# Kernel tuning notes

Measured on AMD Instinct MI355X. Metric: run time of the kernel, lower is better.

Reference implementation:

```python
import jax, jax.numpy as jnp
import numpy as np

B, T, DIM = 4, 1024, 2048
N_HEADS, N_KV_HEADS = 32, 8
HEAD_DIM = DIM // N_HEADS  # 64
N_REPS = N_HEADS // N_KV_HEADS  # 4


def setup_inputs() -> dict:
    key = jax.random.key(0)
    ks = jax.random.split(key, 8)
    # RoPE tables: theta = 10000^{-2i/d}, positions 0..T-1
    inv_freq = 1.0 / (10000.0 ** (jnp.arange(0, HEAD_DIM, 2, dtype=jnp.float32) / HEAD_DIM))
    angles = jnp.arange(T, dtype=jnp.float32)[:, None] * inv_freq[None, :]  # (T, HEAD_DIM//2)
    s = 0.02
    return {
        "input": jax.random.normal(ks[0], (B, T, DIM), jnp.float32),
        "freqs_cos": jnp.cos(angles),
        "freqs_sin": jnp.sin(angles),
        "mask": jnp.tril(jnp.ones((T, T), dtype=bool)),  # causal boolean mask
        "wq": s * jax.random.normal(ks[1], (DIM, DIM), jnp.float32),
        "wk": s * jax.random.normal(ks[2], (N_KV_HEADS * HEAD_DIM, DIM), jnp.float32),
        "wv": s * jax.random.normal(ks[3], (N_KV_HEADS * HEAD_DIM, DIM), jnp.float32),
        "wo": s * jax.random.normal(ks[4], (DIM, DIM), jnp.float32),
        "curr_pos": 0,
    }


def _apply_rope(x, cos, sin):
    # x: (B, T, H, D); cos/sin: (T, D//2). Complex multiply on (even, odd) pairs.
    xr = x[..., 0::2]
    xi = x[..., 1::2]
    c = cos[None, :, None, :]
    s = sin[None, :, None, :]
    out_r = xr * c - xi * s
    out_i = xr * s + xi * c
    return jnp.stack([out_r, out_i], axis=-1).reshape(x.shape)


def reference(input, freqs_cos, freqs_sin, mask, wq, wk, wv, wo, curr_pos):
    Bv, Tv = input.shape[0], input.shape[1]
    qs = (input @ wq.T).reshape(Bv, Tv, N_HEADS, HEAD_DIM)
    ks = (input @ wk.T).reshape(Bv, Tv, N_KV_HEADS, HEAD_DIM)
    vs = (input @ wv.T).reshape(Bv, Tv, N_KV_HEADS, HEAD_DIM)
    qs = _apply_rope(qs, freqs_cos, freqs_sin)
    ks = _apply_rope(ks, freqs_cos, freqs_sin)

    # KV cache (prefill path: curr_pos == 0, fresh cache of length 2T)
    kv_cache = jnp.zeros((Bv, 2 * Tv, N_KV_HEADS, HEAD_DIM, 2), input.dtype)
    kv_cache = kv_cache.at[:, curr_pos:curr_pos + Tv, :, :, 0].set(ks)
    kv_cache = kv_cache.at[:, curr_pos:curr_pos + Tv, :, :, 1].set(vs)
    k_all = kv_cache[:, :curr_pos + Tv, :, :, 0]
    v_all = kv_cache[:, :curr_pos + Tv, :, :, 1]

    # GQA: broadcast each kv head across its query-head group (avoid repeat_interleave copy)
    S = k_all.shape[1]
    q = qs.transpose(0, 2, 1, 3).reshape(Bv, N_KV_HEADS, N_REPS, Tv, HEAD_DIM)
    k = k_all.transpose(0, 2, 1, 3)  # (B, KVH, S, D)
    v = v_all.transpose(0, 2, 1, 3)

    scale = 1.0 / jnp.sqrt(jnp.asarray(HEAD_DIM, input.dtype))
    scores = jnp.einsum("bgrqd,bgkd->bgrqk", q, k) * scale  # (B, KVH, REPS, T, S)
    neg = jnp.asarray(jnp.finfo(input.dtype).min, input.dtype)
    scores = jnp.where(mask[None, None, None, :, :S], scores, neg)
    attn = jax.nn.softmax(scores, axis=-1)
    out = jnp.einsum("bgrqk,bgkd->bgrqd", attn, v)
    out = out.reshape(Bv, N_HEADS, Tv, HEAD_DIM).transpose(0, 2, 1, 3).reshape(Bv, Tv, DIM)
    return out @ wo.T
```

## Files before the change

kernel.cpp:

```cpp
#include <hip/hip_runtime.h>
#include <cstdint>

typedef __bf16 bf16x8 __attribute__((ext_vector_type(8)));
typedef float  f32x4  __attribute__((ext_vector_type(4)));
typedef float  f32x16 __attribute__((ext_vector_type(16)));
typedef float  float8v __attribute__((ext_vector_type(8)));
typedef unsigned short ushort8v __attribute__((ext_vector_type(8)));
typedef unsigned short ushort4v __attribute__((ext_vector_type(4)));
typedef unsigned int   uint4v   __attribute__((ext_vector_type(4)));

__device__ __forceinline__ unsigned short f2b(float f) {
  uint32_t u = __builtin_bit_cast(uint32_t, f);
  u += 0x7FFFu + ((u >> 16) & 1u);
  return (unsigned short)(u >> 16);
}
__device__ __forceinline__ float b2f(unsigned short h) {
  uint32_t u = ((uint32_t)h) << 16;
  return __builtin_bit_cast(float, u);
}
__device__ __forceinline__ unsigned int cvtpk(float lo, float hi_) {
  unsigned int r;
  asm("v_cvt_pk_bf16_f32 %0, %1, %2" : "=v"(r) : "v"(lo), "v"(hi_));
  return r;
}

__device__ __forceinline__ void async16(const void* g, void* l) {
  __builtin_amdgcn_global_load_lds(
      (const __attribute__((address_space(1))) void*)g,
      (__attribute__((address_space(3))) void*)l, 16, 0, 0);
}

#define WAITVM(N)  __builtin_amdgcn_s_waitcnt(0x0F70 | ((N) & 15))

struct CvtArgs {
  const float* src[5];
  unsigned short* dst[5];
  long n[5];
};
__global__ void cvt5_kernel(CvtArgs a) {
  long base = (long)blockIdx.x * blockDim.x + threadIdx.x;
  long gstride = (long)gridDim.x * blockDim.x;
#pragma unroll 1
  for (int sg = 0; sg < 5; ++sg) {
    const float* s = a.src[sg];
    unsigned short* d = a.dst[sg];
    long n8 = a.n[sg] >> 3;
    for (long i = base; i < n8; i += gstride) {
      float8v f = *(const float8v*)(s + i * 8);
      ushort8v o;
#pragma unroll
      for (int j = 0; j < 8; ++j) o[j] = f2b(f[j]);
      *(ushort8v*)(d + i * 8) = o;
    }
  }
}

__global__ __launch_bounds__(512, 2)
void gemmQ192(const unsigned short* __restrict__ Ag, const unsigned short* __restrict__ Wg,
              unsigned short* __restrict__ Cp) {
  constexpr int K = 2048;
  constexpr int NF = 3;
  constexpr int ASLOT = 16384;
  constexpr int BSLOT = 24576;
  constexpr int N = 3072;

  extern __shared__ char lds_c[];

  const int tid = threadIdx.x;
  const int wave = tid >> 6, lane = tid & 63;
  const int wm = wave >> 2, wn = wave & 3;
  const int lr = lane & 15, lg = lane >> 4;

  const int flat = blockIdx.y * 16 + blockIdx.x;
  const int swz = (flat & 7) * 32 + (flat >> 3);
  const int m0 = (swz >> 4) * 256, n0 = (swz & 15) * 192;

  const int laneSw = (lr >> 1) * 128 + (((((lr & 1) << 2) | lg) ^ (lr >> 1)) << 4);
  const int aoff = wm * 8192 + laneSw;

  int bByte[NF], bR7[NF];
#pragma unroll
  for (int ni = 0; ni < NF; ++ni) {
    int row = wn * 48 + ni * 16 + lr;
    bByte[ni] = row * 128;
    bR7[ni] = row & 7;
  }

  f32x4 acc[8][NF] = {};
  bf16x8 af[4], bf[NF];

  auto stA = [&](int slot, int s) {
    char* sl = lds_c + slot * ASLOT;
    const int kc = s * 32;
#pragma unroll
    for (int j = 0; j < 2; ++j) {
      int q = (tid + 512 * j) * 16;
      int R = q >> 7, g2L = ((q >> 4) & 7) ^ (R & 7);
      int row = R * 2 + (g2L >> 2), kg = g2L & 3;
      async16(Ag + (size_t)(m0 + row) * K + kc + kg * 8, sl + q);
    }
  };
  auto stB = [&](int slot, int T) {
    char* sl = lds_c + 4 * ASLOT + slot * BSLOT;
    const int kc = T * 64;
#pragma unroll
    for (int j = 0; j < 3; ++j) {
      int q = (tid + 512 * j) * 16;
      int row = q >> 7, c = (q >> 4) & 7;
      async16(Wg + (size_t)(n0 + row) * K + kc + ((c ^ (row & 7)) * 8), sl + q);
    }
  };

#define PH(SA, SB, MH, KH, RDB, STG, VM)                                      \
  {                                                                           \
    const char* As_ = lds_c + (SA) * ASLOT;                                   \
    _Pragma("unroll") for (int mi = 0; mi < 4; ++mi)                          \
      af[mi] = *(const bf16x8*)(As_ + aoff + ((MH) * 4 + mi) * 1024);         \
    if (RDB) {                                                                \
      const char* Bs_ = lds_c + 4 * ASLOT + (SB) * BSLOT;                     \
      _Pragma("unroll") for (int ni = 0; ni < NF; ++ni)                       \
        bf[ni] = *(const bf16x8*)(Bs_ + bByte[ni] +                           \
                                  (((((KH) << 2) | lg) ^ bR7[ni]) << 4));     \
    }                                                                         \
    STG;                                                                      \
    if ((VM) >= 0) WAITVM(VM);                                                \
    __builtin_amdgcn_s_barrier();                                             \
    __builtin_amdgcn_s_setprio(1);                                            \
    _Pragma("unroll") for (int mi = 0; mi < 4; ++mi)                          \
      _Pragma("unroll") for (int ni = 0; ni < NF; ++ni)                       \
        acc[(MH) * 4 + mi][ni] = __builtin_amdgcn_mfma_f32_16x16x32_bf16(     \
            af[mi], bf[ni], acc[(MH) * 4 + mi][ni], 0, 0, 0);                 \
    __builtin_amdgcn_s_setprio(0);                                            \
    __builtin_amdgcn_s_barrier();                                             \
  }

  stB(0, 0); stA(0, 0); stA(1, 1); stB(1, 1); stA(2, 2);
  WAITVM(5);
  __builtin_amdgcn_s_barrier();

  for (int t2 = 0; t2 < 30; t2 += 2) {
    PH(0, 0, 0, 0, true,  stA(3, 2 * t2 + 3), -1);
    PH(0, 0, 1, 0, false, (void)0, -1);
    PH(1, 0, 0, 1, true,  stA(0, 2 * t2 + 4), -1);
    PH(1, 0, 1, 1, false, stB(0, t2 + 2), 5);
    PH(2, 1, 0, 0, true,  stA(1, 2 * t2 + 5), -1);
    PH(2, 1, 1, 0, false, (void)0, -1);
    PH(3, 1, 0, 1, true,  stA(2, 2 * t2 + 6), -1);
    PH(3, 1, 1, 1, false, stB(1, t2 + 3), 5);
  }
  PH(0, 0, 0, 0, true,  stA(3, 63), -1);
  PH(0, 0, 1, 0, false, (void)0, -1);
  PH(1, 0, 0, 1, true,  (void)0, -1);
  PH(1, 0, 1, 1, false, (void)0, 0);
  PH(2, 1, 0, 0, true,  (void)0, -1);
  PH(2, 1, 1, 0, false, (void)0, -1);
  PH(3, 1, 0, 1, true,  (void)0, -1);
  PH(3, 1, 1, 1, false, (void)0, -1);
#undef PH

#pragma unroll
  for (int mig = 0; mig < 8; ++mig) {
#pragma unroll
    for (int j = 0; j < 4; ++j) {
      int row = m0 + wm * 128 + mig * 16 + lg * 4 + j;
#pragma unroll
      for (int ni = 0; ni < NF; ++ni) {
        int col = n0 + wn * 48 + ni * 16 + lr;
        Cp[(size_t)row * N + col] = f2b(acc[mig][ni][j]);
      }
    }
  }
}

template<bool F32OUT, int BN, int GX, int GY>
__global__ __launch_bounds__(512, 2)
void gemm8p(const unsigned short* __restrict__ Ag, const unsigned short* __restrict__ Wg,
            void* __restrict__ Cp, int N) {
  constexpr int K = 2048;
  constexpr int BM = 256;
  constexpr int NF = BN / 64;
  constexpr int AL = 2;
  constexpr int BL = BN / 128;
  constexpr int VMS = 2 * BL + AL;
  constexpr int ASLOT = BM * 64;
  constexpr int BSLOT = BN * 64;
  constexpr int NWG = GX * GY;
  constexpr int CPX = NWG / 8;

  extern __shared__ char lds_c[];

  const int tid = threadIdx.x;
  const int wave = tid >> 6, lane = tid & 63;
  const int wm = wave >> 2, wn = wave & 3;
  const int lr = lane & 15, lg = lane >> 4;

  const int flat = blockIdx.y * GX + blockIdx.x;
  const int swz = (flat & 7) * CPX + (flat >> 3);
  const int m0 = (swz / GX) * BM, n0 = (swz % GX) * BN;

  const int laneSw = (lr >> 1) * 128 + (((((lr & 1) << 2) | lg) ^ (lr >> 1)) << 4);
  const int aoff = wm * 128 * 64 + laneSw;
  const int boff = wn * NF * 1024 + laneSw;

  f32x4 acc[8][NF] = {};
  bf16x8 af[4], bf[NF];

  auto stA = [&](int slot, int s) {
    char* sl = lds_c + slot * ASLOT;
    const int kc = s * 32;
#pragma unroll
    for (int j = 0; j < AL; ++j) {
      int q = (tid + 512 * j) * 16;
      int R = q >> 7, g2L = ((q >> 4) & 7) ^ (R & 7);
      int row = R * 2 + (g2L >> 2), kg = g2L & 3;
      async16(Ag + (size_t)(m0 + row) * K + kc + kg * 8, sl + q);
    }
  };
  auto stB = [&](int slot, int s) {
    char* sl = lds_c + 4 * ASLOT + slot * BSLOT;
    const int kc = s * 32;
#pragma unroll
    for (int j = 0; j < BL; ++j) {
      int q = (tid + 512 * j) * 16;
      int R = q >> 7, g2L = ((q >> 4) & 7) ^ (R & 7);
      int row = R * 2 + (g2L >> 2), kg = g2L & 3;
      async16(Wg + (size_t)(n0 + row) * K + kc + kg * 8, sl + q);
    }
  };

#define PH(RSLOT, MH, RDB, STG, VM)                                           \
  {                                                                           \
    const char* As_ = lds_c + (RSLOT) * ASLOT;                                \
    _Pragma("unroll") for (int mi = 0; mi < 4; ++mi)                          \
      af[mi] = *(const bf16x8*)(As_ + aoff + ((MH) * 4 + mi) * 1024);         \
    if (RDB) {                                                                \
      const char* Bs_ = lds_c + 4 * ASLOT + (RSLOT) * BSLOT;                  \
      _Pragma("unroll") for (int ni = 0; ni < NF; ++ni)                       \
        bf[ni] = *(const bf16x8*)(Bs_ + boff + ni * 1024);                    \
    }                                                                         \
    STG;                                                                      \
    if ((VM) >= 0) WAITVM(VM);                                                \
    __builtin_amdgcn_s_barrier();                                             \
    __builtin_amdgcn_s_setprio(1);                                            \
    _Pragma("unroll") for (int mi = 0; mi < 4; ++mi)                          \
      _Pragma("unroll") for (int ni = 0; ni < NF; ++ni)                       \
        acc[(MH) * 4 + mi][ni] = __builtin_amdgcn_mfma_f32_16x16x32_bf16(     \
            af[mi], bf[ni], acc[(MH) * 4 + mi][ni], 0, 0, 0);                 \
    __builtin_amdgcn_s_setprio(0);                                            \
    __builtin_amdgcn_s_barrier();                                             \
  }

  stB(0, 0); stA(0, 0); stB(1, 1); stA(1, 1); stB(2, 2); stA(2, 2); stB(3, 3);
  WAITVM(VMS);
  __builtin_amdgcn_s_barrier();

  for (int T = 0; T < 30; T += 2) {
    const int p0 = 2 * T;
    PH(0, 0, true,  stA(3, p0 + 3), -1);
    PH(0, 1, false, stB(0, p0 + 4), -1);
    PH(1, 0, true,  stA(0, p0 + 4), -1);
    PH(1, 1, false, stB(1, p0 + 5), VMS);
    PH(2, 0, true,  stA(1, p0 + 5), -1);
    PH(2, 1, false, stB(2, p0 + 6), -1);
    PH(3, 0, true,  stA(2, p0 + 6), -1);
    PH(3, 1, false, stB(3, p0 + 7), VMS);
  }
  PH(0, 0, true,  stA(3, 63), -1);
  PH(0, 1, false, (void)0, -1);
  PH(1, 0, true,  (void)0, -1);
  PH(1, 1, false, (void)0, 0);
  PH(2, 0, true,  (void)0, -1);
  PH(2, 1, false, (void)0, -1);
  PH(3, 0, true,  (void)0, -1);
  PH(3, 1, false, (void)0, -1);
#undef PH

#pragma unroll
  for (int mig = 0; mig < 8; ++mig) {
#pragma unroll
    for (int j = 0; j < 4; ++j) {
      int row = m0 + wm * 128 + mig * 16 + lg * 4 + j;
#pragma unroll
      for (int ni = 0; ni < NF; ++ni) {
        int col = n0 + wn * (NF * 16) + ni * 16 + lr;
        float v = acc[mig][ni][j];
        if (F32OUT) ((float*)Cp)[(size_t)row * N + col] = v;
        else        ((unsigned short*)Cp)[(size_t)row * N + col] = f2b(v);
      }
    }
  }
}

__global__ __launch_bounds__(256)
void ropekv_kernel(unsigned short* __restrict__ qkv,
                   const float* __restrict__ cosb, const float* __restrict__ sinb,
                   unsigned short* __restrict__ vt) {
  const int tt0 = blockIdx.x * 64;
  const int kvh = blockIdx.y;
  const int b   = blockIdx.z;
  const int tid = threadIdx.x;

  {
    int r = tid >> 2, c0 = (tid & 3) * 16;
    int t = tt0 + r;
    unsigned short* kp = qkv + (size_t)(b * 1024 + t) * 3072 + 2048 + kvh * 64 + c0;
    const float* cb = cosb + t * 32 + c0 / 2;
    const float* sb = sinb + t * 32 + c0 / 2;
    ushort8v x0 = *(const ushort8v*)kp;
    ushort8v x1 = *(const ushort8v*)(kp + 8);
    float8v c = *(const float8v*)cb;
    float8v s = *(const float8v*)sb;
    ushort8v o0, o1;
#pragma unroll
    for (int j = 0; j < 4; ++j) {
      float xr = b2f(x0[2 * j]), xi = b2f(x0[2 * j + 1]);
      o0[2 * j]     = f2b(xr * c[j] - xi * s[j]);
      o0[2 * j + 1] = f2b(xr * s[j] + xi * c[j]);
    }
#pragma unroll
    for (int j = 0; j < 4; ++j) {
      float xr = b2f(x1[2 * j]), xi = b2f(x1[2 * j + 1]);
      o1[2 * j]     = f2b(xr * c[4 + j] - xi * s[4 + j]);
      o1[2 * j + 1] = f2b(xr * s[4 + j] + xi * c[4 + j]);
    }
    *(ushort8v*)kp = o0;
    *(ushort8v*)(kp + 8) = o1;
  }

  __shared__ unsigned short lT[64 * 68];
#pragma unroll
  for (int i = 0; i < 2; ++i) {
    int r = i * 32 + (tid >> 3), c = (tid & 7) * 8;
    const unsigned short* src = qkv + (size_t)(b * 1024 + tt0 + r) * 3072 + 2560 + kvh * 64 + c;
    ushort8v v = *(const ushort8v*)src;
    ushort4v a, b4;
#pragma unroll
    for (int j = 0; j < 4; ++j) { a[j] = v[j]; b4[j] = v[j + 4]; }
    *(ushort4v*)&lT[r * 68 + c]     = a;
    *(ushort4v*)&lT[r * 68 + c + 4] = b4;
  }
  __syncthreads();
#pragma unroll
  for (int i = 0; i < 2; ++i) {
    int d = tid & 63;
    int tt = i * 4 + (tid >> 6);
    ushort8v o;
#pragma unroll
    for (int j = 0; j < 8; ++j) o[j] = lT[(tt * 8 + j) * 68 + d];
    *(ushort8v*)&vt[((size_t)((b * 8 + kvh) * 64 + d)) * 1024 + tt0 + tt * 8] = o;
  }
}

__global__ __launch_bounds__(512, 4)
void attn_kernel(const unsigned short* __restrict__ qkv, const unsigned short* __restrict__ vt,
                 const float* __restrict__ cosb, const float* __restrict__ sinb,
                 unsigned short* __restrict__ ob) {
  const int flat = (blockIdx.z * 8 + blockIdx.y) * 16 + blockIdx.x;
  const int swzb = (flat & 7) * 64 + (flat >> 3);
  const int bx = swzb & 15, kvh = (swzb >> 4) & 7, b = swzb >> 7;

  const int tid = threadIdx.x, wave = tid >> 6, lane = tid & 63;
  const int l31 = lane & 31, hi = lane >> 5;
  const int wq = wave & 3, wh = wave >> 2;
  const int h = kvh * 4 + wq;

  const int qth = 31 - bx, qtl = bx;
  const int nth = qth / 2 + 1, ntl = qtl / 2 + 1;
  const int q0 = (wh ? qtl : qth) * 32;
  const int nt = wh ? ntl : nth;

  __shared__ unsigned short lK[2][64 * 64];
  __shared__ unsigned short lVt[2][64 * 64];

  const float SC = 0.125f * 1.44269504f;
  bf16x8 qf[4];
  {
    int t = q0 + l31;
    const unsigned short* qp = qkv + (size_t)(b * 1024 + t) * 3072 + h * 64;
#pragma unroll
    for (int dk = 0; dk < 4; ++dk) {
      ushort8v q = *(const ushort8v*)(qp + dk * 16 + hi * 8);
      f32x4 c4 = *(const f32x4*)(cosb + t * 32 + dk * 8 + hi * 4);
      f32x4 s4 = *(const f32x4*)(sinb + t * 32 + dk * 8 + hi * 4);
      ushort8v o;
#pragma unroll
      for (int j = 0; j < 4; ++j) {
        float xr = b2f(q[2 * j]), xi = b2f(q[2 * j + 1]);
        o[2 * j]     = f2b((xr * c4[j] - xi * s4[j]) * SC);
        o[2 * j + 1] = f2b((xr * s4[j] + xi * c4[j]) * SC);
      }
      qf[dk] = __builtin_bit_cast(bf16x8, o);
    }
  }

  const unsigned short* kg = qkv + (size_t)(b * 1024) * 3072 + 2048 + kvh * 64;
  const unsigned short* vg = vt + (size_t)(b * 8 + kvh) * 64 * 1024;

  auto stage = [&](int kvb, int bi) {
    const int sr  = tid >> 3;
    const int scb = (tid & 7) * 16;
    {
      int cb = scb ^ ((sr & 7) << 4);
      async16(kg + (size_t)(kvb + sr) * 3072 + (cb >> 1), &lK[bi][sr * 64 + (scb >> 1)]);
    }
    {
      int cbv = scb ^ ((sr & 7) << 4);
      async16(vg + (size_t)sr * 1024 + kvb + (cbv >> 1), &lVt[bi][sr * 64 + (scb >> 1)]);
    }
  };

  f32x16 oacc[2] = {};
  float m2 = -3e38f, l_run = 0.f;

  auto chunk64 = [&](int cur, int ckvb, bool lastT) {
    f32x16 sd[2] = {};
    __builtin_amdgcn_s_setprio(1);
#pragma unroll
    for (int s = 0; s < 2; ++s) {
      const int krow = s * 32 + l31;
      const char* kr = (const char*)lK[cur] + krow * 128;
      const int swz = (krow & 7) << 4;
#pragma unroll
      for (int dk = 0; dk < 4; ++dk) {
        bf16x8 kf = *(const bf16x8*)(kr + ((dk * 32 + hi * 16) ^ swz));
        sd[s] = __builtin_amdgcn_mfma_f32_32x32x16_bf16(kf, qf[dk], sd[s], 0, 0, 0);
      }
    }
    __builtin_amdgcn_s_setprio(0);

    if (lastT) {
#pragma unroll
      for (int s = 0; s < 2; ++s)
#pragma unroll
        for (int r = 0; r < 16; ++r) {
          int kvg = ckvb + s * 32 + (r & 3) + 8 * (r >> 2) + 4 * hi;
          if (kvg > q0 + l31) sd[s][r] = -3e38f;
        }
    }
    float pm = sd[0][0];
#pragma unroll
    for (int s = 0; s < 2; ++s)
#pragma unroll
      for (int r = 0; r < 16; ++r) pm = fmaxf(pm, sd[s][r]);
    pm = fmaxf(pm, __shfl_xor(pm, 32));
    if (!__all(pm <= m2 + 11.0f)) {
      float mnew = fmaxf(m2, pm);
      float alpha = exp2f(m2 - mnew);
      m2 = mnew;
      l_run *= alpha;
#pragma unroll
      for (int db = 0; db < 2; ++db)
#pragma unroll
        for (int r = 0; r < 16; ++r) oacc[db][r] *= alpha;
    }
    float tsum = 0.f;
#pragma unroll
    for (int s = 0; s < 2; ++s)
#pragma unroll
      for (int r = 0; r < 16; ++r) { float p = exp2f(sd[s][r] - m2); sd[s][r] = p; tsum += p; }
    tsum += __shfl_xor(tsum, 32);
    l_run += tsum;

    bf16x8 pf[2][2];
#pragma unroll
    for (int s = 0; s < 2; ++s)
#pragma unroll
      for (int kc = 0; kc < 2; ++kc) {
        unsigned int cA = cvtpk(sd[s][8 * kc + 0], sd[s][8 * kc + 1]);
        unsigned int cB = cvtpk(sd[s][8 * kc + 4], sd[s][8 * kc + 5]);
        unsigned int cC = cvtpk(sd[s][8 * kc + 2], sd[s][8 * kc + 3]);
        unsigned int cD = cvtpk(sd[s][8 * kc + 6], sd[s][8 * kc + 7]);
        unsigned int xA = __shfl_xor(cA, 32), xB = __shfl_xor(cB, 32);
        unsigned int xC = __shfl_xor(cC, 32), xD = __shfl_xor(cD, 32);
        uint4v u;
        u[0] = hi ? xB : cA;
        u[1] = hi ? xD : cC;
        u[2] = hi ? cB : xA;
        u[3] = hi ? cD : xC;
        pf[s][kc] = __builtin_bit_cast(bf16x8, u);
      }

    __builtin_amdgcn_s_setprio(1);
#pragma unroll
    for (int db = 0; db < 2; ++db) {
      const int row = db * 32 + l31;
      const char* vr = (const char*)lVt[cur] + row * 128;
      const int vswz = (row & 7) << 4;
#pragma unroll
      for (int s = 0; s < 2; ++s)
#pragma unroll
        for (int kc = 0; kc < 2; ++kc) {
          bf16x8 vf = *(const bf16x8*)(vr + ((s * 64 + kc * 32 + hi * 16) ^ vswz));
          oacc[db] = __builtin_amdgcn_mfma_f32_32x32x16_bf16(vf, pf[s][kc], oacc[db], 0, 0, 0);
        }
    }
    __builtin_amdgcn_s_setprio(0);
  };

  stage(0, 0);
  __syncthreads();

  for (int j = 0; j < nth; ++j) {
    const int cur = j & 1;
    if (j + 1 < nth) stage((j + 1) * 64, cur ^ 1);
    if (j < nt) chunk64(cur, j * 64, j == nt - 1);
    __syncthreads();
  }

  {
    float inv = 1.0f / l_run;
    unsigned short* orow = ob + (size_t)(b * 1024 + q0 + l31) * 2048 + h * 64;
#pragma unroll
    for (int db = 0; db < 2; ++db)
#pragma unroll
      for (int g = 0; g < 4; ++g) {
        int d0 = db * 32 + 8 * g + 4 * hi;
        ushort4v o;
#pragma unroll
        for (int j = 0; j < 4; ++j) o[j] = f2b(oacc[db][4 * g + j] * inv);
        *(ushort4v*)(orow + d0) = o;
      }
  }
}

extern "C" void kernel_launch(void* const* d_in, const int* in_sizes, int n_in,
                              void* d_out, int out_size, void* d_ws, size_t ws_size,
                              hipStream_t stream) {
  const float* input = (const float*)d_in[0];
  const float* fcos  = (const float*)d_in[1];
  const float* fsin  = (const float*)d_in[2];
  const float* wq = (const float*)d_in[4];
  const float* wk = (const float*)d_in[5];
  const float* wv = (const float*)d_in[6];
  const float* wo = (const float*)d_in[7];
  float* out = (float*)d_out;

  unsigned short* xb   = (unsigned short*)d_ws;
  unsigned short* wqkv = xb + (size_t)4096 * 2048;
  unsigned short* wob  = wqkv + (size_t)3072 * 2048;
  unsigned short* qkv  = wob + (size_t)2048 * 2048;
  unsigned short* ob   = qkv + (size_t)4096 * 3072;
  unsigned short* vtb  = xb;

  hipFuncSetAttribute((const void*)&gemmQ192,
                      hipFuncAttributeMaxDynamicSharedMemorySize, 114688);
  hipFuncSetAttribute((const void*)&gemm8p<true, 128, 16, 16>,
                      hipFuncAttributeMaxDynamicSharedMemorySize, 98304);

  CvtArgs ca;
  ca.src[0] = input; ca.dst[0] = xb;                        ca.n[0] = (long)4096 * 2048;
  ca.src[1] = wq;    ca.dst[1] = wqkv;                      ca.n[1] = (long)2048 * 2048;
  ca.src[2] = wk;    ca.dst[2] = wqkv + (size_t)2048 * 2048; ca.n[2] = (long)512 * 2048;
  ca.src[3] = wv;    ca.dst[3] = wqkv + (size_t)2560 * 2048; ca.n[3] = (long)512 * 2048;
  ca.src[4] = wo;    ca.dst[4] = wob;                       ca.n[4] = (long)2048 * 2048;
  hipLaunchKernelGGL(cvt5_kernel, dim3(2048), dim3(256), 0, stream, ca);

  hipLaunchKernelGGL(gemmQ192, dim3(16, 16), dim3(512), 114688,
                     stream, xb, wqkv, qkv);

  hipLaunchKernelGGL(ropekv_kernel, dim3(16, 8, 4), dim3(256), 0, stream,
                     qkv, fcos, fsin, vtb);

  hipLaunchKernelGGL(attn_kernel, dim3(16, 8, 4), dim3(512), 0, stream,
                     qkv, vtb, fcos, fsin, ob);

  hipLaunchKernelGGL((gemm8p<true, 128, 16, 16>), dim3(16, 16), dim3(512), 98304,
                     stream, ob, wob, (void*)out, 2048);
}
```

Baseline: 157.0 us.

## Halve GEMM M-tile to 128 rows and unify both projections in one template

Replaces the QKV GEMM and the output GEMM with one templated kernel that uses 128-row tiles instead of 256, doubling the grid to 512 workgroups. LDS per block drops and launch bounds go to 4 blocks per CU, so more waves can hide latency and the 256 CUs get better wave coverage. In exchange, per-block operand reuse falls and B-tile traffic per FLOP doubles. The output GEMM also moves from its old pipeline variant to the QKV-style B-loading scheme.

```diff
diff --git a/kernel.cpp b/kernel.cpp
--- a/kernel.cpp
+++ b/kernel.cpp
@@ -55,14 +55,17 @@
   }
 }
 
-__global__ __launch_bounds__(512, 2)
-void gemmQ192(const unsigned short* __restrict__ Ag, const unsigned short* __restrict__ Wg,
-              unsigned short* __restrict__ Cp) {
+template<bool F32OUT, int BN>
+__global__ __launch_bounds__(512, 4)
+void gemmLT(const unsigned short* __restrict__ Ag, const unsigned short* __restrict__ Wg,
+            void* __restrict__ Cp) {
   constexpr int K = 2048;
-  constexpr int NF = 3;
-  constexpr int ASLOT = 16384;
-  constexpr int BSLOT = 24576;
-  constexpr int N = 3072;
+  constexpr int NF = BN / 64;
+  constexpr int BL = NF;
+  constexpr int VMS = 1 + BL;
+  constexpr int ASLOT = 8192;
+  constexpr int BSLOT = BN * 128;
+  constexpr int N = 16 * BN;
 
   extern __shared__ char lds_c[];
 
@@ -72,39 +75,36 @@
   const int lr = lane & 15, lg = lane >> 4;
 
   const int flat = blockIdx.y * 16 + blockIdx.x;
-  const int swz = (flat & 7) * 32 + (flat >> 3);
-  const int m0 = (swz >> 4) * 256, n0 = (swz & 15) * 192;
+  const int swz = (flat & 7) * 64 + (flat >> 3);
+  const int m0 = (swz >> 4) * 128, n0 = (swz & 15) * BN;
 
   const int laneSw = (lr >> 1) * 128 + (((((lr & 1) << 2) | lg) ^ (lr >> 1)) << 4);
-  const int aoff = wm * 8192 + laneSw;
+  const int aoff = wm * 4096 + laneSw;
 
   int bByte[NF], bR7[NF];
 #pragma unroll
   for (int ni = 0; ni < NF; ++ni) {
-    int row = wn * 48 + ni * 16 + lr;
+    int row = wn * (NF * 16) + ni * 16 + lr;
     bByte[ni] = row * 128;
     bR7[ni] = row & 7;
   }
 
-  f32x4 acc[8][NF] = {};
-  bf16x8 af[4], bf[NF];
+  f32x4 acc[4][NF] = {};
+  bf16x8 af[2], bf[NF];
 
   auto stA = [&](int slot, int s) {
     char* sl = lds_c + slot * ASLOT;
     const int kc = s * 32;
-#pragma unroll
-    for (int j = 0; j < 2; ++j) {
-      int q = (tid + 512 * j) * 16;
-      int R = q >> 7, g2L = ((q >> 4) & 7) ^ (R & 7);
-      int row = R * 2 + (g2L >> 2), kg = g2L & 3;
-      async16(Ag + (size_t)(m0 + row) * K + kc + kg * 8, sl + q);
-    }
+    int q = tid * 16;
+    int R = q >> 7, g2L = ((q >> 4) & 7) ^ (R & 7);
+    int row = R * 2 + (g2L >> 2), kg = g2L & 3;
+    async16(Ag + (size_t)(m0 + row) * K + kc + kg * 8, sl + q);
   };
   auto stB = [&](int slot, int T) {
     char* sl = lds_c + 4 * ASLOT + slot * BSLOT;
     const int kc = T * 64;
 #pragma unroll
-    for (int j = 0; j < 3; ++j) {
+    for (int j = 0; j < BL; ++j) {
       int q = (tid + 512 * j) * 16;
       int row = q >> 7, c = (q >> 4) & 7;
       async16(Wg + (size_t)(n0 + row) * K + kc + ((c ^ (row & 7)) * 8), sl + q);
@@ -114,8 +114,8 @@
 #define PH(SA, SB, MH, KH, RDB, STG, VM)                                      \
   {                                                                           \
     const char* As_ = lds_c + (SA) * ASLOT;                                   \
-    _Pragma("unroll") for (int mi = 0; mi < 4; ++mi)                          \
-      af[mi] = *(const bf16x8*)(As_ + aoff + ((MH) * 4 + mi) * 1024);         \
+    _Pragma("unroll") for (int mi = 0; mi < 2; ++mi)                          \
+      af[mi] = *(const bf16x8*)(As_ + aoff + ((MH) * 2 + mi) * 1024);         \
     if (RDB) {                                                                \
       const char* Bs_ = lds_c + 4 * ASLOT + (SB) * BSLOT;                     \
       _Pragma("unroll") for (int ni = 0; ni < NF; ++ni)                       \
@@ -126,27 +126,27 @@
     if ((VM) >= 0) WAITVM(VM);                                                \
     __builtin_amdgcn_s_barrier();                                             \
     __builtin_amdgcn_s_setprio(1);                                            \
-    _Pragma("unroll") for (int mi = 0; mi < 4; ++mi)                          \
+    _Pragma("unroll") for (int mi = 0; mi < 2; ++mi)                          \
       _Pragma("unroll") for (int ni = 0; ni < NF; ++ni)                       \
-        acc[(MH) * 4 + mi][ni] = __builtin_amdgcn_mfma_f32_16x16x32_bf16(     \
-            af[mi], bf[ni], acc[(MH) * 4 + mi][ni], 0, 0, 0);                 \
+        acc[(MH) * 2 + mi][ni] = __builtin_amdgcn_mfma_f32_16x16x32_bf16(     \
+            af[mi], bf[ni], acc[(MH) * 2 + mi][ni], 0, 0, 0);                 \
     __builtin_amdgcn_s_setprio(0);                                            \
     __builtin_amdgcn_s_barrier();                                             \
   }
 
   stB(0, 0); stA(0, 0); stA(1, 1); stB(1, 1); stA(2, 2);
-  WAITVM(5);
+  WAITVM(VMS);
   __builtin_amdgcn_s_barrier();
 
   for (int t2 = 0; t2 < 30; t2 += 2) {
     PH(0, 0, 0, 0, true,  stA(3, 2 * t2 + 3), -1);
     PH(0, 0, 1, 0, false, (void)0, -1);
     PH(1, 0, 0, 1, true,  stA(0, 2 * t2 + 4), -1);
-    PH(1, 0, 1, 1, false, stB(0, t2 + 2), 5);
+    PH(1, 0, 1, 1, false, stB(0, t2 + 2), VMS);
     PH(2, 1, 0, 0, true,  stA(1, 2 * t2 + 5), -1);
     PH(2, 1, 1, 0, false, (void)0, -1);
     PH(3, 1, 0, 1, true,  stA(2, 2 * t2 + 6), -1);
-    PH(3, 1, 1, 1, false, stB(1, t2 + 3), 5);
+    PH(3, 1, 1, 1, false, stB(1, t2 + 3), VMS);
   }
   PH(0, 0, 0, 0, true,  stA(3, 63), -1);
   PH(0, 0, 1, 0, false, (void)0, -1);
@@ -159,127 +159,10 @@
 #undef PH
 
 #pragma unroll
-  for (int mig = 0; mig < 8; ++mig) {
+  for (int mig = 0; mig < 4; ++mig) {
 #pragma unroll
     for (int j = 0; j < 4; ++j) {
-      int row = m0 + wm * 128 + mig * 16 + lg * 4 + j;
-#pragma unroll
-      for (int ni = 0; ni < NF; ++ni) {
-        int col = n0 + wn * 48 + ni * 16 + lr;
-        Cp[(size_t)row * N + col] = f2b(acc[mig][ni][j]);
-      }
-    }
-  }
-}
-
-template<bool F32OUT, int BN, int GX, int GY>
-__global__ __launch_bounds__(512, 2)
-void gemm8p(const unsigned short* __restrict__ Ag, const unsigned short* __restrict__ Wg,
-            void* __restrict__ Cp, int N) {
-  constexpr int K = 2048;
-  constexpr int BM = 256;
-  constexpr int NF = BN / 64;
-  constexpr int AL = 2;
-  constexpr int BL = BN / 128;
-  constexpr int VMS = 2 * BL + AL;
-  constexpr int ASLOT = BM * 64;
-  constexpr int BSLOT = BN * 64;
-  constexpr int NWG = GX * GY;
-  constexpr int CPX = NWG / 8;
-
-  extern __shared__ char lds_c[];
-
-  const int tid = threadIdx.x;
-  const int wave = tid >> 6, lane = tid & 63;
-  const int wm = wave >> 2, wn = wave & 3;
-  const int lr = lane & 15, lg = lane >> 4;
-
-  const int flat = blockIdx.y * GX + blockIdx.x;
-  const int swz = (flat & 7) * CPX + (flat >> 3);
-  const int m0 = (swz / GX) * BM, n0 = (swz % GX) * BN;
-
-  const int laneSw = (lr >> 1) * 128 + (((((lr & 1) << 2) | lg) ^ (lr >> 1)) << 4);
-  const int aoff = wm * 128 * 64 + laneSw;
-  const int boff = wn * NF * 1024 + laneSw;
-
-  f32x4 acc[8][NF] = {};
-  bf16x8 af[4], bf[NF];
-
-  auto stA = [&](int slot, int s) {
-    char* sl = lds_c + slot * ASLOT;
-    const int kc = s * 32;
-#pragma unroll
-    for (int j = 0; j < AL; ++j) {
-      int q = (tid + 512 * j) * 16;
-      int R = q >> 7, g2L = ((q >> 4) & 7) ^ (R & 7);
-      int row = R * 2 + (g2L >> 2), kg = g2L & 3;
-      async16(Ag + (size_t)(m0 + row) * K + kc + kg * 8, sl + q);
-    }
-  };
-  auto stB = [&](int slot, int s) {
-    char* sl = lds_c + 4 * ASLOT + slot * BSLOT;
-    const int kc = s * 32;
-#pragma unroll
-    for (int j = 0; j < BL; ++j) {
-      int q = (tid + 512 * j) * 16;
-      int R = q >> 7, g2L = ((q >> 4) & 7) ^ (R & 7);
-      int row = R * 2 + (g2L >> 2), kg = g2L & 3;
-      async16(Wg + (size_t)(n0 + row) * K + kc + kg * 8, sl + q);
-    }
-  };
-
-#define PH(RSLOT, MH, RDB, STG, VM)                                           \
-  {                                                                           \
-    const char* As_ = lds_c + (RSLOT) * ASLOT;                                \
-    _Pragma("unroll") for (int mi = 0; mi < 4; ++mi)                          \
-      af[mi] = *(const bf16x8*)(As_ + aoff + ((MH) * 4 + mi) * 1024);         \
-    if (RDB) {                                                                \
-      const char* Bs_ = lds_c + 4 * ASLOT + (RSLOT) * BSLOT;                  \
-      _Pragma("unroll") for (int ni = 0; ni < NF; ++ni)                       \
-        bf[ni] = *(const bf16x8*)(Bs_ + boff + ni * 1024);                    \
-    }                                                                         \
-    STG;                                                                      \
-    if ((VM) >= 0) WAITVM(VM);                                                \
-    __builtin_amdgcn_s_barrier();                                             \
-    __builtin_amdgcn_s_setprio(1);                                            \
-    _Pragma("unroll") for (int mi = 0; mi < 4; ++mi)                          \
-      _Pragma("unroll") for (int ni = 0; ni < NF; ++ni)                       \
-        acc[(MH) * 4 + mi][ni] = __builtin_amdgcn_mfma_f32_16x16x32_bf16(     \
-            af[mi], bf[ni], acc[(MH) * 4 + mi][ni], 0, 0, 0);                 \
-    __builtin_amdgcn_s_setprio(0);                                            \
-    __builtin_amdgcn_s_barrier();                                             \
-  }
-
-  stB(0, 0); stA(0, 0); stB(1, 1); stA(1, 1); stB(2, 2); stA(2, 2); stB(3, 3);
-  WAITVM(VMS);
-  __builtin_amdgcn_s_barrier();
-
-  for (int T = 0; T < 30; T += 2) {
-    const int p0 = 2 * T;
-    PH(0, 0, true,  stA(3, p0 + 3), -1);
-    PH(0, 1, false, stB(0, p0 + 4), -1);
-    PH(1, 0, true,  stA(0, p0 + 4), -1);
-    PH(1, 1, false, stB(1, p0 + 5), VMS);
-    PH(2, 0, true,  stA(1, p0 + 5), -1);
-    PH(2, 1, false, stB(2, p0 + 6), -1);
-    PH(3, 0, true,  stA(2, p0 + 6), -1);
-    PH(3, 1, false, stB(3, p0 + 7), VMS);
-  }
-  PH(0, 0, true,  stA(3, 63), -1);
-  PH(0, 1, false, (void)0, -1);
-  PH(1, 0, true,  (void)0, -1);
-  PH(1, 1, false, (void)0, 0);
-  PH(2, 0, true,  (void)0, -1);
-  PH(2, 1, false, (void)0, -1);
-  PH(3, 0, true,  (void)0, -1);
-  PH(3, 1, false, (void)0, -1);
-#undef PH
-
-#pragma unroll
-  for (int mig = 0; mig < 8; ++mig) {
-#pragma unroll
-    for (int j = 0; j < 4; ++j) {
-      int row = m0 + wm * 128 + mig * 16 + lg * 4 + j;
+      int row = m0 + wm * 64 + mig * 16 + lg * 4 + j;
 #pragma unroll
       for (int ni = 0; ni < NF; ++ni) {
         int col = n0 + wn * (NF * 16) + ni * 16 + lr;
@@ -542,10 +425,10 @@
   unsigned short* ob   = qkv + (size_t)4096 * 3072;
   unsigned short* vtb  = xb;
 
-  hipFuncSetAttribute((const void*)&gemmQ192,
-                      hipFuncAttributeMaxDynamicSharedMemorySize, 114688);
-  hipFuncSetAttribute((const void*)&gemm8p<true, 128, 16, 16>,
-                      hipFuncAttributeMaxDynamicSharedMemorySize, 98304);
+  hipFuncSetAttribute((const void*)&gemmLT<false, 192>,
+                      hipFuncAttributeMaxDynamicSharedMemorySize, 81920);
+  hipFuncSetAttribute((const void*)&gemmLT<true, 128>,
+                      hipFuncAttributeMaxDynamicSharedMemorySize, 65536);
 
   CvtArgs ca;
   ca.src[0] = input; ca.dst[0] = xb;                        ca.n[0] = (long)4096 * 2048;
@@ -555,8 +438,8 @@
   ca.src[4] = wo;    ca.dst[4] = wob;                       ca.n[4] = (long)2048 * 2048;
   hipLaunchKernelGGL(cvt5_kernel, dim3(2048), dim3(256), 0, stream, ca);
 
-  hipLaunchKernelGGL(gemmQ192, dim3(16, 16), dim3(512), 114688,
-                     stream, xb, wqkv, qkv);
+  hipLaunchKernelGGL((gemmLT<false, 192>), dim3(16, 32), dim3(512), 81920,
+                     stream, xb, wqkv, (void*)qkv);
 
   hipLaunchKernelGGL(ropekv_kernel, dim3(16, 8, 4), dim3(256), 0, stream,
                      qkv, fcos, fsin, vtb);
@@ -564,6 +447,6 @@
   hipLaunchKernelGGL(attn_kernel, dim3(16, 8, 4), dim3(512), 0, stream,
                      qkv, vtb, fcos, fsin, ob);
 
-  hipLaunchKernelGGL((gemm8p<true, 128, 16, 16>), dim3(16, 16), dim3(512), 98304,
-                     stream, ob, wob, (void*)out, 2048);
-}
+  hipLaunchKernelGGL((gemmLT<true, 128>), dim3(16, 32), dim3(512), 65536,
+                     stream, ob, wob, (void*)out);
+}
```

After: 158.2 us, median of 2. Within noise of the previous version (+0.7%).
